# Performance work log

Measured on AMD Instinct MI355X. Metric: run time of the kernel, lower is better.

## Reference

```python
import jax, jax.numpy as jnp
import numpy as np

B, L, D = 4, 2048, 2048
NH, HD, K = 32, 64, 16
LR = 1.0
EPS = 1e-6


def ln_fwd(x, gamma, beta):
    mu = x.mean(-1, keepdims=True)
    var = jnp.var(x, axis=-1, keepdims=True)
    x_hat = (x - mu) / jnp.sqrt(var + EPS)
    return gamma * x_hat + beta


def ln_fused_l2_bwd(x, target, gamma, beta):
    # grad of 0.5*||LN(x)-target||^2 wrt x (matches LayerNormFunction.backward
    # with grad_output = LN(x) - target)
    d = x.shape[-1]
    mu = x.mean(-1, keepdims=True)
    var = jnp.var(x, axis=-1, keepdims=True)
    std = jnp.sqrt(var + EPS)
    x_hat = (x - mu) / std
    y = gamma * x_hat + beta
    g = (y - target) * gamma
    return (d * g - g.sum(-1, keepdims=True) - x_hat * (g * x_hat).sum(-1, keepdims=True)) / (d * std)


def setup_inputs() -> dict:
    key = jax.random.key(0)
    ks = jax.random.split(key, 12)
    s = 0.02
    return {
        "hidden_states": jax.random.normal(ks[0], (B, L, D), jnp.float32),
        "Wq": jax.random.normal(ks[1], (D, D), jnp.float32) * s,
        "Wk": jax.random.normal(ks[2], (D, D), jnp.float32) * s,
        "Wv": jax.random.normal(ks[3], (D, D), jnp.float32) * s,
        "Wo": jax.random.normal(ks[4], (D, D), jnp.float32) * s,
        "linear_weight": jax.random.normal(ks[5], (NH, 1, D), jnp.float32) * s,
        "linear_bias": jnp.zeros((NH, 1), jnp.float32),
        "ln_weight": jnp.ones((NH, HD), jnp.float32),
        "ln_bias": jnp.zeros((NH, HD), jnp.float32),
        "W1_init": jax.random.normal(ks[6], (NH, HD, HD), jnp.float32) * s,
        "b1_init": jnp.zeros((NH, 1, HD), jnp.float32),
    }


def reference(hidden_states, Wq, Wk, Wv, Wo, linear_weight, linear_bias,
              ln_weight, ln_bias, W1_init, b1_init):
    Bq, Lq, Dq = hidden_states.shape
    n_chunk = Lq // K

    def split(x):  # [B,L,D] -> [B,NH,n_chunk,K,HD]
        return x.reshape(Bq, n_chunk, K, NH, HD).transpose(0, 3, 1, 2, 4)

    XC = split(hidden_states @ Wq.T)
    XB = split(hidden_states @ Wk.T)
    XA = split(hidden_states @ Wv.T)

    # inner-loop learning-rate coefficient: [B,NH,n_chunk,K,1]
    X = hidden_states.reshape(Bq, n_chunk, K, Dq)
    ilr = jnp.einsum('bnkd,hd->bhnk', X, linear_weight[:, 0, :]) + linear_bias[:, 0][None, :, None, None]
    ilr_gated = jax.nn.sigmoid(ilr)[..., None]
    token_idx = 1.0 / jnp.arange(1, K + 1, dtype=hidden_states.dtype)
    coeff = (LR * token_idx).reshape(1, 1, 1, K, 1) * ilr_gated / HD

    ln_w = ln_weight.reshape(1, NH, 1, HD)
    ln_b = ln_bias.reshape(1, NH, 1, HD)
    mask = jnp.tril(jnp.ones((K, K), hidden_states.dtype))

    W1 = jnp.broadcast_to(W1_init[None], (Bq, NH, HD, HD))
    b1 = jnp.broadcast_to(b1_init[None], (Bq, NH, 1, HD))

    def step(carry, inp):
        W1, b1 = carry
        xc, xb, xa, co = inp  # [B,NH,K,HD], co: [B,NH,K,1]
        Z1 = xb @ W1 + b1
        grad = ln_fused_l2_bwd(Z1, xa - xb, ln_w, ln_b)  # [B,NH,K,HD]
        Attn = mask * jnp.einsum('bhkf,bhjf->bhkj', xc, xb)
        E = mask * co.transpose(0, 1, 3, 2)  # E[i,j] = coeff_j * (j<=i)
        b1_bar = b1 - E @ grad
        Z1_bar = xc @ W1 - (Attn * E) @ grad + b1_bar
        W1_new = W1 - jnp.einsum('bhkf,bhkg->bhfg', co * xb, grad)
        b1_new = b1 - (co * grad).sum(-2, keepdims=True)
        out = xc + ln_fwd(Z1_bar, ln_w, ln_b)
        return (W1_new, b1_new), out

    xs = (XC.transpose(2, 0, 1, 3, 4), XB.transpose(2, 0, 1, 3, 4),
          XA.transpose(2, 0, 1, 3, 4), coeff.transpose(2, 0, 1, 3, 4))
    (_, _), outs = jax.lax.scan(step, (W1, b1), xs)
    # outs: [n_chunk,B,NH,K,HD] -> [B,L,D]
    XCW = outs.transpose(1, 0, 3, 2, 4).reshape(Bq, Lq, Dq)
    return XCW @ Wo.T
```

## Files before the change

kernel.cpp:

```cpp
#include <hip/hip_runtime.h>


typedef __attribute__((ext_vector_type(4))) float float4v;
typedef __attribute__((ext_vector_type(8))) __bf16 bf16x8;
typedef __attribute__((ext_vector_type(4))) short short4v;
typedef __attribute__((ext_vector_type(4))) unsigned int uint4v;
typedef __attribute__((ext_vector_type(2))) unsigned int uint2v;

__device__ __forceinline__ unsigned short f2bf(float f) {
  unsigned int u = __builtin_bit_cast(unsigned int, f);
  u += 0x7FFFu + ((u >> 16) & 1u);
  return (unsigned short)(u >> 16);
}
__device__ __forceinline__ float bf2f(unsigned short s) {
  unsigned int u = ((unsigned int)s) << 16;
  return __builtin_bit_cast(float, u);
}
__device__ __forceinline__ void lds_load16(const void* g, void* l) {
  __builtin_amdgcn_global_load_lds((const __attribute__((address_space(1))) void*)g,
                                   (__attribute__((address_space(3))) void*)l, 16, 0, 0);
}

__device__ __forceinline__ void store_out(float* p, float v) { *p = v; }
__device__ __forceinline__ void store_out(unsigned short* p, float v) { *p = f2bf(v); }

template <int CTRL>
__device__ __forceinline__ float dppmov(float x) {
  return __builtin_bit_cast(
      float, __builtin_amdgcn_update_dpp(0, __builtin_bit_cast(int, x), CTRL, 0xF, 0xF, true));
}
__device__ __forceinline__ float red16(float x) {
  x += dppmov<0xB1>(x);
  x += dppmov<0x4E>(x);
  x += dppmov<0x124>(x);
  x += dppmov<0x128>(x);
  return x;
}
__device__ __forceinline__ unsigned int cvtpk_bf16(float lo, float hi) {
  unsigned int r;
  asm("v_cvt_pk_bf16_f32 %0, %1, %2" : "=v"(r) : "v"(lo), "v"(hi));
  return r;
}

template <typename OUT>
__global__ __launch_bounds__(256) void gemm_bt(
    const unsigned short* __restrict__ A, const unsigned short* __restrict__ B,
    OUT* __restrict__ C, int M, int N, int K) {
  __shared__ unsigned short sA[128 * 32];
  __shared__ unsigned short sB[128 * 32];
  const int tid = threadIdx.x;
  const int wave = tid >> 6;
  const int lane = tid & 63;
  const int quad = lane >> 4;
  const int l15 = lane & 15;
  const int wm = (wave >> 1) * 64;
  const int wn = (wave & 1) * 64;
  const int bm = blockIdx.y * 128;
  const int bn = blockIdx.x * 128;

  float4v acc[4][4];
#pragma unroll
  for (int i = 0; i < 4; ++i)
#pragma unroll
    for (int j = 0; j < 4; ++j) acc[i][j] = (float4v){0.f, 0.f, 0.f, 0.f};

  const int srow = tid >> 2;
  const int scol = (tid & 3) * 8;
  const unsigned short* aptr = A + (size_t)(bm + srow) * K + scol;
  const unsigned short* bptr = B + (size_t)(bn + srow) * K + scol;
  unsigned short* sAw0 = &sA[wave * 512];
  unsigned short* sAw1 = &sA[2048 + wave * 512];
  unsigned short* sBw0 = &sB[wave * 512];
  unsigned short* sBw1 = &sB[2048 + wave * 512];
  const size_t astep = (size_t)64 * K;

  for (int kt = 0; kt < K; kt += 32) {
    __syncthreads();
    lds_load16(aptr + kt, sAw0);
    lds_load16(aptr + kt + astep, sAw1);
    lds_load16(bptr + kt, sBw0);
    lds_load16(bptr + kt + astep, sBw1);
    __syncthreads();
    bf16x8 af[4], bf[4];
#pragma unroll
    for (int i = 0; i < 4; ++i)
      af[i] = *(const bf16x8*)&sA[(wm + i * 16 + l15) * 32 + quad * 8];
#pragma unroll
    for (int j = 0; j < 4; ++j)
      bf[j] = *(const bf16x8*)&sB[(wn + j * 16 + l15) * 32 + quad * 8];
#pragma unroll
    for (int i = 0; i < 4; ++i)
#pragma unroll
      for (int j = 0; j < 4; ++j)
        acc[i][j] = __builtin_amdgcn_mfma_f32_16x16x32_bf16(af[i], bf[j], acc[i][j], 0, 0, 0);
  }

#pragma unroll
  for (int i = 0; i < 4; ++i) {
    const int row0 = bm + wm + i * 16 + quad * 4;
#pragma unroll
    for (int j = 0; j < 4; ++j) {
      const int col = bn + wn + j * 16 + l15;
#pragma unroll
      for (int r = 0; r < 4; ++r)
        store_out(&C[(size_t)(row0 + r) * N + col], acc[i][j][r]);
    }
  }
}

__global__ __launch_bounds__(256) void f32_to_bf16_k(const float* __restrict__ s,
                                                     unsigned short* __restrict__ d, int n) {
  const int i = (blockIdx.x * 256 + threadIdx.x) * 8;
  if (i >= n) return;
  const float4v a = *(const float4v*)(s + i);
  const float4v b = *(const float4v*)(s + i + 4);
  uint4v o;
  o[0] = (unsigned int)f2bf(a[0]) | ((unsigned int)f2bf(a[1]) << 16);
  o[1] = (unsigned int)f2bf(a[2]) | ((unsigned int)f2bf(a[3]) << 16);
  o[2] = (unsigned int)f2bf(b[0]) | ((unsigned int)f2bf(b[1]) << 16);
  o[3] = (unsigned int)f2bf(b[2]) | ((unsigned int)f2bf(b[3]) << 16);
  *(uint4v*)(d + i) = o;
}

__global__ __launch_bounds__(256) void coeff_k(const unsigned short* __restrict__ ilr,
                                               const float* __restrict__ lb,
                                               float* __restrict__ coeff) {
  const int gid = blockIdx.x * 256 + threadIdx.x;
  const int row = gid >> 5;
  const int h = gid & 31;
  const float v = bf2f(ilr[row * 128 + h]) + lb[h];
  const float sig = 1.0f / (1.0f + __expf(-v));
  const int b = row >> 11;
  const int pos = row & 2047;
  const int cc = pos >> 4;
  const int k = pos & 15;
  coeff[((((size_t)b * 32 + h) * 128 + cc) << 4) + k] = sig / (64.0f * (float)(k + 1));
}

__global__ __launch_bounds__(64, 1) void ttt_scan(
    const unsigned short* __restrict__ XC, const unsigned short* __restrict__ XB,
    const unsigned short* __restrict__ XA, const float* __restrict__ coeff,
    const float* __restrict__ lnw, const float* __restrict__ lnb,
    const float* __restrict__ W1i, const float* __restrict__ b1i,
    unsigned short* __restrict__ XCW) {
  const int b = blockIdx.x >> 5;
  const int h = blockIdx.x & 31;
  const int lane = threadIdx.x;
  const int quad = lane >> 4;
  const int l15 = lane & 15;

  constexpr int LDW = 88;
  __shared__ unsigned short sW1[64 * LDW];
  __shared__ unsigned short sXC[16 * LDW];
  __shared__ unsigned short sXB[16 * LDW];
  __shared__ unsigned short sXA[16 * LDW];

  float gam[4], bet[4];
#pragma unroll
  for (int nt = 0; nt < 4; ++nt) {
    gam[nt] = lnw[h * 64 + nt * 16 + l15];
    bet[nt] = lnb[h * 64 + nt * 16 + l15];
  }
  float4v W1r[16];
#pragma unroll
  for (int mt = 0; mt < 4; ++mt)
#pragma unroll
    for (int nt = 0; nt < 4; ++nt) {
      float4v v;
#pragma unroll
      for (int r = 0; r < 4; ++r)
        v[r] = W1i[(size_t)h * 4096 + (size_t)(mt * 16 + quad * 4 + r) * 64 + nt * 16 + l15];
      W1r[mt * 4 + nt] = v;
    }
  float b1v[4];
#pragma unroll
  for (int nt = 0; nt < 4; ++nt) b1v[nt] = b1i[h * 64 + nt * 16 + l15];

  const int srow = lane >> 2;
  const int scol = (lane & 3) * 16;
  const size_t hdoff = (size_t)h * 64;
  const size_t browoff = (size_t)b * 2048;
  const float* cobase = coeff + (((size_t)b * 32 + h) * 128) * 16;
  const float inv64 = 1.0f / 64.0f;
  const float4v zero4 = {0.f, 0.f, 0.f, 0.f};

  uint4v pxc0, pxc1, pxb0, pxb1, pxa0, pxa1;
  float4v pcof;
  {
    const size_t goff = (browoff + (size_t)srow) * 2048 + hdoff + scol;
    pxc0 = *(const uint4v*)(XC + goff);
    pxc1 = *(const uint4v*)(XC + goff + 8);
    pxb0 = *(const uint4v*)(XB + goff);
    pxb1 = *(const uint4v*)(XB + goff + 8);
    pxa0 = *(const uint4v*)(XA + goff);
    pxa1 = *(const uint4v*)(XA + goff + 8);
    pcof = *(const float4v*)(cobase + quad * 4);
  }

  for (int c = 0; c < 128; ++c) {
    const uint4v xc0 = pxc0, xc1 = pxc1, xb0 = pxb0, xb1 = pxb1, xa0 = pxa0, xa1 = pxa1;
    const float4v cof = pcof;
    {
      const int cn = (c < 127) ? c + 1 : 127;
      const size_t goff = (browoff + (size_t)(cn * 16 + srow)) * 2048 + hdoff + scol;
      pxc0 = *(const uint4v*)(XC + goff);
      pxc1 = *(const uint4v*)(XC + goff + 8);
      pxb0 = *(const uint4v*)(XB + goff);
      pxb1 = *(const uint4v*)(XB + goff + 8);
      pxa0 = *(const uint4v*)(XA + goff);
      pxa1 = *(const uint4v*)(XA + goff + 8);
      pcof = *(const float4v*)(cobase + (size_t)cn * 16 + quad * 4);
    }

    *(uint4v*)&sXC[srow * LDW + scol] = xc0;
    *(uint4v*)&sXC[srow * LDW + scol + 8] = xc1;
    *(uint4v*)&sXB[srow * LDW + scol] = xb0;
    *(uint4v*)&sXB[srow * LDW + scol + 8] = xb1;
    *(uint4v*)&sXA[srow * LDW + scol] = xa0;
    *(uint4v*)&sXA[srow * LDW + scol + 8] = xa1;

#pragma unroll
    for (int mt = 0; mt < 4; ++mt)
#pragma unroll
      for (int nt = 0; nt < 4; ++nt) {
        const float4v w = W1r[mt * 4 + nt];
        uint2v p;
        p[0] = cvtpk_bf16(w[0], w[1]);
        p[1] = cvtpk_bf16(w[2], w[3]);
        *(uint2v*)&sW1[(nt * 16 + l15) * LDW + mt * 16 + quad * 4] = p;
      }

    bf16x8 xbf[2], xcf[2];
#pragma unroll
    for (int hh = 0; hh < 2; ++hh) {
      xbf[hh] = *(const bf16x8*)&sXB[l15 * LDW + hh * 32 + quad * 8];
      xcf[hh] = *(const bf16x8*)&sXC[l15 * LDW + hh * 32 + quad * 8];
    }
    bf16x8 w1f[4][2];
#pragma unroll
    for (int nt = 0; nt < 4; ++nt)
#pragma unroll
      for (int hh = 0; hh < 2; ++hh)
        w1f[nt][hh] = *(const bf16x8*)&sW1[(nt * 16 + l15) * LDW + hh * 32 + quad * 8];

    float4v at = __builtin_amdgcn_mfma_f32_16x16x32_bf16(xbf[0], xcf[0], zero4, 0, 0, 0);
    at = __builtin_amdgcn_mfma_f32_16x16x32_bf16(xbf[1], xcf[1], at, 0, 0, 0);

    float4v z[4];
#pragma unroll
    for (int nt = 0; nt < 4; ++nt) {
      float4v t = __builtin_amdgcn_mfma_f32_16x16x32_bf16(xbf[0], w1f[nt][0], zero4, 0, 0, 0);
      t = __builtin_amdgcn_mfma_f32_16x16x32_bf16(xbf[1], w1f[nt][1], t, 0, 0, 0);
#pragma unroll
      for (int r = 0; r < 4; ++r) t[r] += b1v[nt];
      z[nt] = t;
    }

    float s1[4], s2[4];
#pragma unroll
    for (int r = 0; r < 4; ++r) {
      s1[r] = red16(z[0][r] + z[1][r] + z[2][r] + z[3][r]);
      s2[r] = red16(z[0][r] * z[0][r] + z[1][r] * z[1][r] + z[2][r] * z[2][r] +
                    z[3][r] * z[3][r]);
    }
    float mu[4], rstd[4];
#pragma unroll
    for (int r = 0; r < 4; ++r) {
      mu[r] = s1[r] * inv64;
      const float var = s2[r] * inv64 - mu[r] * mu[r];
      rstd[r] = rsqrtf(var + 1e-6f);
    }
    float xh[4][4], gg[4][4];
#pragma unroll
    for (int nt = 0; nt < 4; ++nt)
#pragma unroll
      for (int r = 0; r < 4; ++r) {
        const float xhat = (z[nt][r] - mu[r]) * rstd[r];
        xh[nt][r] = xhat;
        const float y = gam[nt] * xhat + bet[nt];
        const int toff = (quad * 4 + r) * LDW + nt * 16 + l15;
        const float tgt = bf2f(sXA[toff]) - bf2f(sXB[toff]);
        gg[nt][r] = (y - tgt) * gam[nt];
      }
    float sg[4], sgx[4];
#pragma unroll
    for (int r = 0; r < 4; ++r) {
      sg[r] = red16(gg[0][r] + gg[1][r] + gg[2][r] + gg[3][r]);
      sgx[r] = red16(gg[0][r] * xh[0][r] + gg[1][r] * xh[1][r] + gg[2][r] * xh[2][r] +
                     gg[3][r] * xh[3][r]);
    }
    float grad[4][4];
    short4v gradb[4];
#pragma unroll
    for (int nt = 0; nt < 4; ++nt)
#pragma unroll
      for (int r = 0; r < 4; ++r) {
        grad[nt][r] = (64.0f * gg[nt][r] - sg[r] - xh[nt][r] * sgx[r]) * (rstd[r] * inv64);
        gradb[nt][r] = (short)f2bf(grad[nt][r]);
      }

    short4v m1f;
#pragma unroll
    for (int jj = 0; jj < 4; ++jj) {
      const int k = quad * 4 + jj;
      const float e = (k <= l15) ? cof[jj] : 0.0f;
      m1f[jj] = (short)f2bf(-(at[jj] + 1.0f) * e);
    }

#pragma unroll
    for (int nt = 0; nt < 4; ++nt) {
      float4v t = __builtin_amdgcn_mfma_f32_16x16x32_bf16(xcf[0], w1f[nt][0], zero4, 0, 0, 0);
      t = __builtin_amdgcn_mfma_f32_16x16x32_bf16(xcf[1], w1f[nt][1], t, 0, 0, 0);
      t = __builtin_amdgcn_mfma_f32_16x16x16bf16_1k(m1f, gradb[nt], t, 0, 0, 0);
#pragma unroll
      for (int r = 0; r < 4; ++r) t[r] += b1v[nt];
      z[nt] = t;
    }

#pragma unroll
    for (int r = 0; r < 4; ++r) {
      s1[r] = red16(z[0][r] + z[1][r] + z[2][r] + z[3][r]);
      s2[r] = red16(z[0][r] * z[0][r] + z[1][r] * z[1][r] + z[2][r] * z[2][r] +
                    z[3][r] * z[3][r]);
    }
#pragma unroll
    for (int r = 0; r < 4; ++r) {
      mu[r] = s1[r] * inv64;
      const float var = s2[r] * inv64 - mu[r] * mu[r];
      rstd[r] = rsqrtf(var + 1e-6f);
    }
#pragma unroll
    for (int nt = 0; nt < 4; ++nt)
#pragma unroll
      for (int r = 0; r < 4; ++r) {
        const float xhat = (z[nt][r] - mu[r]) * rstd[r];
        const float y = gam[nt] * xhat + bet[nt];
        const float o = bf2f(sXC[(quad * 4 + r) * LDW + nt * 16 + l15]) + y;
        XCW[(browoff + (size_t)(c * 16 + quad * 4 + r)) * 2048 + hdoff + nt * 16 + l15] = f2bf(o);
      }

#pragma unroll
    for (int nt = 0; nt < 4; ++nt) {
      float pb = cof[0] * grad[nt][0] + cof[1] * grad[nt][1] + cof[2] * grad[nt][2] +
                 cof[3] * grad[nt][3];
      pb += __shfl_xor(pb, 16);
      pb += __shfl_xor(pb, 32);
      b1v[nt] -= pb;
    }

#pragma unroll
    for (int mt = 0; mt < 4; ++mt) {
      short4v caf;
#pragma unroll
      for (int jj = 0; jj < 4; ++jj)
        caf[jj] = (short)f2bf(-cof[jj] * bf2f(sXB[(quad * 4 + jj) * LDW + mt * 16 + l15]));
#pragma unroll
      for (int nt = 0; nt < 4; ++nt)
        W1r[mt * 4 + nt] =
            __builtin_amdgcn_mfma_f32_16x16x16bf16_1k(caf, gradb[nt], W1r[mt * 4 + nt], 0, 0, 0);
    }
  }
}

extern "C" void kernel_launch(void* const* d_in, const int* in_sizes, int n_in,
                              void* d_out, int out_size, void* d_ws, size_t ws_size,
                              hipStream_t stream) {
  const float* hs = (const float*)d_in[0];
  const float* Wq = (const float*)d_in[1];
  const float* Wk = (const float*)d_in[2];
  const float* Wv = (const float*)d_in[3];
  const float* Wo = (const float*)d_in[4];
  const float* lw = (const float*)d_in[5];
  const float* lb = (const float*)d_in[6];
  const float* lnw = (const float*)d_in[7];
  const float* lnb = (const float*)d_in[8];
  const float* W1i = (const float*)d_in[9];
  const float* b1i = (const float*)d_in[10];
  float* out = (float*)d_out;
  char* ws = (char*)d_ws;

  unsigned short* hsb = (unsigned short*)(ws);
  unsigned short* wqb = (unsigned short*)(ws + 33554432);
  unsigned short* wkb = (unsigned short*)(ws + 41943040);
  unsigned short* wvb = (unsigned short*)(ws + 50331648);
  unsigned short* wob = (unsigned short*)(ws + 58720256);
  unsigned short* lwb = (unsigned short*)(ws + 67108864);
  unsigned short* XCb = (unsigned short*)(ws + 67633152);
  unsigned short* XBb = (unsigned short*)(ws + 101187584);
  unsigned short* XAb = (unsigned short*)(ws + 134742016);
  unsigned short* ilrb = (unsigned short*)(ws + 168296448);
  float* coeff = (float*)(ws + 170393600);

  f32_to_bf16_k<<<8192, 256, 0, stream>>>(hs, hsb, 16777216);
  f32_to_bf16_k<<<2048, 256, 0, stream>>>(Wq, wqb, 4194304);
  f32_to_bf16_k<<<2048, 256, 0, stream>>>(Wk, wkb, 4194304);
  f32_to_bf16_k<<<2048, 256, 0, stream>>>(Wv, wvb, 4194304);
  f32_to_bf16_k<<<2048, 256, 0, stream>>>(Wo, wob, 4194304);
  hipMemsetAsync(lwb, 0, 524288, stream);
  f32_to_bf16_k<<<32, 256, 0, stream>>>(lw, lwb, 65536);

  dim3 blk(256);
  dim3 gbig(16, 64);
  gemm_bt<unsigned short><<<gbig, blk, 0, stream>>>(hsb, wqb, XCb, 8192, 2048, 2048);
  gemm_bt<unsigned short><<<gbig, blk, 0, stream>>>(hsb, wkb, XBb, 8192, 2048, 2048);
  gemm_bt<unsigned short><<<gbig, blk, 0, stream>>>(hsb, wvb, XAb, 8192, 2048, 2048);
  gemm_bt<unsigned short><<<dim3(1, 64), blk, 0, stream>>>(hsb, lwb, ilrb, 8192, 128, 2048);
  coeff_k<<<1024, 256, 0, stream>>>(ilrb, lb, coeff);
  ttt_scan<<<128, 64, 0, stream>>>(XCb, XBb, XAb, coeff, lnw, lnb, W1i, b1i, hsb);
  gemm_bt<float><<<gbig, blk, 0, stream>>>(hsb, wob, out, 8192, 2048, 2048);
}
```

Measured before the change: 1.012 ms.

## Split TTT scan across four waves per head with LDS cross-wave reductions

The sequential TTT scan kernel now runs each (batch, head) block with four waves instead of one. Each wave owns a 16-column slice of the 64-wide feature dimension, so W1 state and MFMA work are divided four ways. LayerNorm row statistics are combined across waves through a small shared-memory reduction buffer, which adds three block barriers per chunk. Input tiles are double-buffered in LDS. The aim is to shorten the latency-bound serial chain per chunk, at the cost of barrier synchronisation overhead.

```diff
diff --git a/kernel.cpp b/kernel.cpp
--- a/kernel.cpp
+++ b/kernel.cpp
@@ -2,6 +2,7 @@
 
 
 typedef __attribute__((ext_vector_type(4))) float float4v;
+typedef __attribute__((ext_vector_type(2))) float float2v;
 typedef __attribute__((ext_vector_type(8))) __bf16 bf16x8;
 typedef __attribute__((ext_vector_type(4))) short short4v;
 typedef __attribute__((ext_vector_type(4))) unsigned int uint4v;
@@ -40,6 +41,11 @@
   unsigned int r;
   asm("v_cvt_pk_bf16_f32 %0, %1, %2" : "=v"(r) : "v"(lo), "v"(hi));
   return r;
+}
+__device__ __forceinline__ void bar_sync() {
+  asm volatile("s_waitcnt lgkmcnt(0)" ::: "memory");
+  __builtin_amdgcn_s_barrier();
+  asm volatile("" ::: "memory");
 }
 
 template <typename OUT>
@@ -137,7 +143,7 @@
   coeff[((((size_t)b * 32 + h) * 128 + cc) << 4) + k] = sig / (64.0f * (float)(k + 1));
 }
 
-__global__ __launch_bounds__(64, 1) void ttt_scan(
+__global__ __launch_bounds__(256, 1) void ttt_scan(
     const unsigned short* __restrict__ XC, const unsigned short* __restrict__ XB,
     const unsigned short* __restrict__ XA, const float* __restrict__ coeff,
     const float* __restrict__ lnw, const float* __restrict__ lnb,
@@ -145,160 +151,154 @@
     unsigned short* __restrict__ XCW) {
   const int b = blockIdx.x >> 5;
   const int h = blockIdx.x & 31;
-  const int lane = threadIdx.x;
+  const int tid = threadIdx.x;
+  const int wave = tid >> 6;
+  const int lane = tid & 63;
   const int quad = lane >> 4;
   const int l15 = lane & 15;
 
   constexpr int LDW = 88;
-  __shared__ unsigned short sW1[64 * LDW];
-  __shared__ unsigned short sXC[16 * LDW];
-  __shared__ unsigned short sXB[16 * LDW];
-  __shared__ unsigned short sXA[16 * LDW];
-
-  float gam[4], bet[4];
-#pragma unroll
-  for (int nt = 0; nt < 4; ++nt) {
-    gam[nt] = lnw[h * 64 + nt * 16 + l15];
-    bet[nt] = lnb[h * 64 + nt * 16 + l15];
-  }
-  float4v W1r[16];
-#pragma unroll
-  for (int mt = 0; mt < 4; ++mt)
-#pragma unroll
-    for (int nt = 0; nt < 4; ++nt) {
-      float4v v;
-#pragma unroll
-      for (int r = 0; r < 4; ++r)
-        v[r] = W1i[(size_t)h * 4096 + (size_t)(mt * 16 + quad * 4 + r) * 64 + nt * 16 + l15];
-      W1r[mt * 4 + nt] = v;
-    }
-  float b1v[4];
-#pragma unroll
-  for (int nt = 0; nt < 4; ++nt) b1v[nt] = b1i[h * 64 + nt * 16 + l15];
-
-  const int srow = lane >> 2;
-  const int scol = (lane & 3) * 16;
+  __shared__ __attribute__((aligned(16))) unsigned short sXC[2][16 * LDW];
+  __shared__ __attribute__((aligned(16))) unsigned short sXB[2][16 * LDW];
+  __shared__ __attribute__((aligned(16))) unsigned short sXA[2][16 * LDW];
+  __shared__ __attribute__((aligned(16))) unsigned short sW1[64 * LDW];
+  __shared__ __attribute__((aligned(16))) float sRed[3][16][8];
+
+  const int fcol = wave * 16 + l15;
+  const float gam = lnw[h * 64 + fcol];
+  const float bet = lnb[h * 64 + fcol];
+
+  float4v W1r[4];
+#pragma unroll
+  for (int mt = 0; mt < 4; ++mt) {
+    float4v v;
+#pragma unroll
+    for (int r = 0; r < 4; ++r)
+      v[r] = W1i[(size_t)h * 4096 + (size_t)(mt * 16 + quad * 4 + r) * 64 + fcol];
+    W1r[mt] = v;
+  }
+  float b1v = b1i[h * 64 + fcol];
+
+#pragma unroll
+  for (int mt = 0; mt < 4; ++mt) {
+    uint2v p;
+    p[0] = cvtpk_bf16(W1r[mt][0], W1r[mt][1]);
+    p[1] = cvtpk_bf16(W1r[mt][2], W1r[mt][3]);
+    *(uint2v*)&sW1[(size_t)fcol * LDW + mt * 16 + quad * 4] = p;
+  }
+
+  const int u = tid & 127;
+  const int grow = u >> 3;
+  const int gcol = (u & 7) * 8;
   const size_t hdoff = (size_t)h * 64;
   const size_t browoff = (size_t)b * 2048;
   const float* cobase = coeff + (((size_t)b * 32 + h) * 128) * 16;
   const float inv64 = 1.0f / 64.0f;
   const float4v zero4 = {0.f, 0.f, 0.f, 0.f};
 
-  uint4v pxc0, pxc1, pxb0, pxb1, pxa0, pxa1;
+  uint4v pA = {0, 0, 0, 0}, pB = {0, 0, 0, 0};
   float4v pcof;
   {
-    const size_t goff = (browoff + (size_t)srow) * 2048 + hdoff + scol;
-    pxc0 = *(const uint4v*)(XC + goff);
-    pxc1 = *(const uint4v*)(XC + goff + 8);
-    pxb0 = *(const uint4v*)(XB + goff);
-    pxb1 = *(const uint4v*)(XB + goff + 8);
-    pxa0 = *(const uint4v*)(XA + goff);
-    pxa1 = *(const uint4v*)(XA + goff + 8);
+    const size_t goff = (browoff + (size_t)grow) * 2048 + hdoff + gcol;
+    if (tid < 128) {
+      pA = *(const uint4v*)(XC + goff);
+      pB = *(const uint4v*)(XA + goff);
+    } else {
+      pA = *(const uint4v*)(XB + goff);
+    }
     pcof = *(const float4v*)(cobase + quad * 4);
   }
 
   for (int c = 0; c < 128; ++c) {
-    const uint4v xc0 = pxc0, xc1 = pxc1, xb0 = pxb0, xb1 = pxb1, xa0 = pxa0, xa1 = pxa1;
+    const int buf = c & 1;
+    if (tid < 128) {
+      *(uint4v*)&sXC[buf][grow * LDW + gcol] = pA;
+      *(uint4v*)&sXA[buf][grow * LDW + gcol] = pB;
+    } else {
+      *(uint4v*)&sXB[buf][grow * LDW + gcol] = pA;
+    }
     const float4v cof = pcof;
+    bar_sync();
+
     {
       const int cn = (c < 127) ? c + 1 : 127;
-      const size_t goff = (browoff + (size_t)(cn * 16 + srow)) * 2048 + hdoff + scol;
-      pxc0 = *(const uint4v*)(XC + goff);
-      pxc1 = *(const uint4v*)(XC + goff + 8);
-      pxb0 = *(const uint4v*)(XB + goff);
-      pxb1 = *(const uint4v*)(XB + goff + 8);
-      pxa0 = *(const uint4v*)(XA + goff);
-      pxa1 = *(const uint4v*)(XA + goff + 8);
+      const size_t goff = (browoff + (size_t)(cn * 16 + grow)) * 2048 + hdoff + gcol;
+      if (tid < 128) {
+        pA = *(const uint4v*)(XC + goff);
+        pB = *(const uint4v*)(XA + goff);
+      } else {
+        pA = *(const uint4v*)(XB + goff);
+      }
       pcof = *(const float4v*)(cobase + (size_t)cn * 16 + quad * 4);
     }
 
-    *(uint4v*)&sXC[srow * LDW + scol] = xc0;
-    *(uint4v*)&sXC[srow * LDW + scol + 8] = xc1;
-    *(uint4v*)&sXB[srow * LDW + scol] = xb0;
-    *(uint4v*)&sXB[srow * LDW + scol + 8] = xb1;
-    *(uint4v*)&sXA[srow * LDW + scol] = xa0;
-    *(uint4v*)&sXA[srow * LDW + scol + 8] = xa1;
-
-#pragma unroll
-    for (int mt = 0; mt < 4; ++mt)
-#pragma unroll
-      for (int nt = 0; nt < 4; ++nt) {
-        const float4v w = W1r[mt * 4 + nt];
-        uint2v p;
-        p[0] = cvtpk_bf16(w[0], w[1]);
-        p[1] = cvtpk_bf16(w[2], w[3]);
-        *(uint2v*)&sW1[(nt * 16 + l15) * LDW + mt * 16 + quad * 4] = p;
-      }
-
-    bf16x8 xbf[2], xcf[2];
+    bf16x8 xbf[2], xcf[2], w1f[2];
 #pragma unroll
     for (int hh = 0; hh < 2; ++hh) {
-      xbf[hh] = *(const bf16x8*)&sXB[l15 * LDW + hh * 32 + quad * 8];
-      xcf[hh] = *(const bf16x8*)&sXC[l15 * LDW + hh * 32 + quad * 8];
-    }
-    bf16x8 w1f[4][2];
-#pragma unroll
-    for (int nt = 0; nt < 4; ++nt)
-#pragma unroll
-      for (int hh = 0; hh < 2; ++hh)
-        w1f[nt][hh] = *(const bf16x8*)&sW1[(nt * 16 + l15) * LDW + hh * 32 + quad * 8];
+      xbf[hh] = *(const bf16x8*)&sXB[buf][l15 * LDW + hh * 32 + quad * 8];
+      xcf[hh] = *(const bf16x8*)&sXC[buf][l15 * LDW + hh * 32 + quad * 8];
+      w1f[hh] = *(const bf16x8*)&sW1[(size_t)fcol * LDW + hh * 32 + quad * 8];
+    }
+
+    float4v z = __builtin_amdgcn_mfma_f32_16x16x32_bf16(xbf[0], w1f[0], zero4, 0, 0, 0);
+    z = __builtin_amdgcn_mfma_f32_16x16x32_bf16(xbf[1], w1f[1], z, 0, 0, 0);
+#pragma unroll
+    for (int r = 0; r < 4; ++r) z[r] += b1v;
+
+    float s1p[4], s2p[4];
+#pragma unroll
+    for (int r = 0; r < 4; ++r) {
+      s1p[r] = red16(z[r]);
+      s2p[r] = red16(z[r] * z[r]);
+    }
+    if (l15 == 0) {
+#pragma unroll
+      for (int r = 0; r < 4; ++r)
+        *(float2v*)&sRed[0][quad * 4 + r][wave * 2] = (float2v){s1p[r], s2p[r]};
+    }
 
     float4v at = __builtin_amdgcn_mfma_f32_16x16x32_bf16(xbf[0], xcf[0], zero4, 0, 0, 0);
     at = __builtin_amdgcn_mfma_f32_16x16x32_bf16(xbf[1], xcf[1], at, 0, 0, 0);
 
-    float4v z[4];
-#pragma unroll
-    for (int nt = 0; nt < 4; ++nt) {
-      float4v t = __builtin_amdgcn_mfma_f32_16x16x32_bf16(xbf[0], w1f[nt][0], zero4, 0, 0, 0);
-      t = __builtin_amdgcn_mfma_f32_16x16x32_bf16(xbf[1], w1f[nt][1], t, 0, 0, 0);
-#pragma unroll
-      for (int r = 0; r < 4; ++r) t[r] += b1v[nt];
-      z[nt] = t;
-    }
-
-    float s1[4], s2[4];
-#pragma unroll
-    for (int r = 0; r < 4; ++r) {
-      s1[r] = red16(z[0][r] + z[1][r] + z[2][r] + z[3][r]);
-      s2[r] = red16(z[0][r] * z[0][r] + z[1][r] * z[1][r] + z[2][r] * z[2][r] +
-                    z[3][r] * z[3][r]);
-    }
+    bar_sync();
+
     float mu[4], rstd[4];
 #pragma unroll
     for (int r = 0; r < 4; ++r) {
-      mu[r] = s1[r] * inv64;
-      const float var = s2[r] * inv64 - mu[r] * mu[r];
-      rstd[r] = rsqrtf(var + 1e-6f);
-    }
-    float xh[4][4], gg[4][4];
-#pragma unroll
-    for (int nt = 0; nt < 4; ++nt)
-#pragma unroll
-      for (int r = 0; r < 4; ++r) {
-        const float xhat = (z[nt][r] - mu[r]) * rstd[r];
-        xh[nt][r] = xhat;
-        const float y = gam[nt] * xhat + bet[nt];
-        const int toff = (quad * 4 + r) * LDW + nt * 16 + l15;
-        const float tgt = bf2f(sXA[toff]) - bf2f(sXB[toff]);
-        gg[nt][r] = (y - tgt) * gam[nt];
-      }
-    float sg[4], sgx[4];
-#pragma unroll
-    for (int r = 0; r < 4; ++r) {
-      sg[r] = red16(gg[0][r] + gg[1][r] + gg[2][r] + gg[3][r]);
-      sgx[r] = red16(gg[0][r] * xh[0][r] + gg[1][r] * xh[1][r] + gg[2][r] * xh[2][r] +
-                     gg[3][r] * xh[3][r]);
-    }
-    float grad[4][4];
-    short4v gradb[4];
-#pragma unroll
-    for (int nt = 0; nt < 4; ++nt)
-#pragma unroll
-      for (int r = 0; r < 4; ++r) {
-        grad[nt][r] = (64.0f * gg[nt][r] - sg[r] - xh[nt][r] * sgx[r]) * (rstd[r] * inv64);
-        gradb[nt][r] = (short)f2bf(grad[nt][r]);
-      }
-
+      const float4v v0 = *(const float4v*)&sRed[0][quad * 4 + r][0];
+      const float4v v1 = *(const float4v*)&sRed[0][quad * 4 + r][4];
+      const float s1 = v0[0] + v0[2] + v1[0] + v1[2];
+      const float s2 = v0[1] + v0[3] + v1[1] + v1[3];
+      mu[r] = s1 * inv64;
+      rstd[r] = rsqrtf(s2 * inv64 - mu[r] * mu[r] + 1e-6f);
+    }
+    float xh[4], gg[4];
+#pragma unroll
+    for (int r = 0; r < 4; ++r) {
+      xh[r] = (z[r] - mu[r]) * rstd[r];
+      const int toff = (quad * 4 + r) * LDW + fcol;
+      const float tgt = bf2f(sXA[buf][toff]) - bf2f(sXB[buf][toff]);
+      gg[r] = (gam * xh[r] + bet - tgt) * gam;
+    }
+    float sgp[4], sgxp[4];
+#pragma unroll
+    for (int r = 0; r < 4; ++r) {
+      sgp[r] = red16(gg[r]);
+      sgxp[r] = red16(gg[r] * xh[r]);
+    }
+    if (l15 == 0) {
+#pragma unroll
+      for (int r = 0; r < 4; ++r)
+        *(float2v*)&sRed[1][quad * 4 + r][wave * 2] = (float2v){sgp[r], sgxp[r]};
+    }
+
+    short4v caf[4];
+#pragma unroll
+    for (int mt = 0; mt < 4; ++mt)
+#pragma unroll
+      for (int jj = 0; jj < 4; ++jj)
+        caf[mt][jj] =
+            (short)f2bf(-cof[jj] * bf2f(sXB[buf][(quad * 4 + jj) * LDW + mt * 16 + l15]));
     short4v m1f;
 #pragma unroll
     for (int jj = 0; jj < 4; ++jj) {
@@ -307,57 +307,69 @@
       m1f[jj] = (short)f2bf(-(at[jj] + 1.0f) * e);
     }
 
-#pragma unroll
-    for (int nt = 0; nt < 4; ++nt) {
-      float4v t = __builtin_amdgcn_mfma_f32_16x16x32_bf16(xcf[0], w1f[nt][0], zero4, 0, 0, 0);
-      t = __builtin_amdgcn_mfma_f32_16x16x32_bf16(xcf[1], w1f[nt][1], t, 0, 0, 0);
-      t = __builtin_amdgcn_mfma_f32_16x16x16bf16_1k(m1f, gradb[nt], t, 0, 0, 0);
-#pragma unroll
-      for (int r = 0; r < 4; ++r) t[r] += b1v[nt];
-      z[nt] = t;
-    }
-
-#pragma unroll
-    for (int r = 0; r < 4; ++r) {
-      s1[r] = red16(z[0][r] + z[1][r] + z[2][r] + z[3][r]);
-      s2[r] = red16(z[0][r] * z[0][r] + z[1][r] * z[1][r] + z[2][r] * z[2][r] +
-                    z[3][r] * z[3][r]);
-    }
-#pragma unroll
-    for (int r = 0; r < 4; ++r) {
-      mu[r] = s1[r] * inv64;
-      const float var = s2[r] * inv64 - mu[r] * mu[r];
-      rstd[r] = rsqrtf(var + 1e-6f);
-    }
-#pragma unroll
-    for (int nt = 0; nt < 4; ++nt)
-#pragma unroll
-      for (int r = 0; r < 4; ++r) {
-        const float xhat = (z[nt][r] - mu[r]) * rstd[r];
-        const float y = gam[nt] * xhat + bet[nt];
-        const float o = bf2f(sXC[(quad * 4 + r) * LDW + nt * 16 + l15]) + y;
-        XCW[(browoff + (size_t)(c * 16 + quad * 4 + r)) * 2048 + hdoff + nt * 16 + l15] = f2bf(o);
-      }
-
-#pragma unroll
-    for (int nt = 0; nt < 4; ++nt) {
-      float pb = cof[0] * grad[nt][0] + cof[1] * grad[nt][1] + cof[2] * grad[nt][2] +
-                 cof[3] * grad[nt][3];
+    bar_sync();
+
+    float grad[4];
+    short4v gradb;
+#pragma unroll
+    for (int r = 0; r < 4; ++r) {
+      const float4v v0 = *(const float4v*)&sRed[1][quad * 4 + r][0];
+      const float4v v1 = *(const float4v*)&sRed[1][quad * 4 + r][4];
+      const float sg = v0[0] + v0[2] + v1[0] + v1[2];
+      const float sgx = v0[1] + v0[3] + v1[1] + v1[3];
+      grad[r] = (64.0f * gg[r] - sg - xh[r] * sgx) * (rstd[r] * inv64);
+      gradb[r] = (short)f2bf(grad[r]);
+    }
+
+    float4v zb = __builtin_amdgcn_mfma_f32_16x16x32_bf16(xcf[0], w1f[0], zero4, 0, 0, 0);
+    zb = __builtin_amdgcn_mfma_f32_16x16x32_bf16(xcf[1], w1f[1], zb, 0, 0, 0);
+    zb = __builtin_amdgcn_mfma_f32_16x16x16bf16_1k(m1f, gradb, zb, 0, 0, 0);
+#pragma unroll
+    for (int r = 0; r < 4; ++r) zb[r] += b1v;
+
+#pragma unroll
+    for (int r = 0; r < 4; ++r) {
+      s1p[r] = red16(zb[r]);
+      s2p[r] = red16(zb[r] * zb[r]);
+    }
+    if (l15 == 0) {
+#pragma unroll
+      for (int r = 0; r < 4; ++r)
+        *(float2v*)&sRed[2][quad * 4 + r][wave * 2] = (float2v){s1p[r], s2p[r]};
+    }
+
+    {
+      float pb = cof[0] * grad[0] + cof[1] * grad[1] + cof[2] * grad[2] + cof[3] * grad[3];
       pb += __shfl_xor(pb, 16);
       pb += __shfl_xor(pb, 32);
-      b1v[nt] -= pb;
+      b1v -= pb;
+    }
+#pragma unroll
+    for (int mt = 0; mt < 4; ++mt)
+      W1r[mt] = __builtin_amdgcn_mfma_f32_16x16x16bf16_1k(caf[mt], gradb, W1r[mt], 0, 0, 0);
+
+    bar_sync();
+
+#pragma unroll
+    for (int r = 0; r < 4; ++r) {
+      const float4v v0 = *(const float4v*)&sRed[2][quad * 4 + r][0];
+      const float4v v1 = *(const float4v*)&sRed[2][quad * 4 + r][4];
+      const float s1 = v0[0] + v0[2] + v1[0] + v1[2];
+      const float s2 = v0[1] + v0[3] + v1[1] + v1[3];
+      const float mu2 = s1 * inv64;
+      const float rstd2 = rsqrtf(s2 * inv64 - mu2 * mu2 + 1e-6f);
+      const float xhat = (zb[r] - mu2) * rstd2;
+      const float y = gam * xhat + bet;
+      const float o = bf2f(sXC[buf][(quad * 4 + r) * LDW + fcol]) + y;
+      XCW[(browoff + (size_t)(c * 16 + quad * 4 + r)) * 2048 + hdoff + fcol] = f2bf(o);
     }
 
 #pragma unroll
     for (int mt = 0; mt < 4; ++mt) {
-      short4v caf;
-#pragma unroll
-      for (int jj = 0; jj < 4; ++jj)
-        caf[jj] = (short)f2bf(-cof[jj] * bf2f(sXB[(quad * 4 + jj) * LDW + mt * 16 + l15]));
-#pragma unroll
-      for (int nt = 0; nt < 4; ++nt)
-        W1r[mt * 4 + nt] =
-            __builtin_amdgcn_mfma_f32_16x16x16bf16_1k(caf, gradb[nt], W1r[mt * 4 + nt], 0, 0, 0);
+      uint2v p;
+      p[0] = cvtpk_bf16(W1r[mt][0], W1r[mt][1]);
+      p[1] = cvtpk_bf16(W1r[mt][2], W1r[mt][3]);
+      *(uint2v*)&sW1[(size_t)fcol * LDW + mt * 16 + quad * 4] = p;
     }
   }
 }
@@ -406,6 +418,6 @@
   gemm_bt<unsigned short><<<gbig, blk, 0, stream>>>(hsb, wvb, XAb, 8192, 2048, 2048);
   gemm_bt<unsigned short><<<dim3(1, 64), blk, 0, stream>>>(hsb, lwb, ilrb, 8192, 128, 2048);
   coeff_k<<<1024, 256, 0, stream>>>(ilrb, lb, coeff);
-  ttt_scan<<<128, 64, 0, stream>>>(XCb, XBb, XAb, coeff, lnw, lnb, W1i, b1i, hsb);
+  ttt_scan<<<128, 256, 0, stream>>>(XCb, XBb, XAb, coeff, lnw, lnb, W1i, b1i, hsb);
   gemm_bt<float><<<gbig, blk, 0, stream>>>(hsb, wob, out, 8192, 2048, 2048);
 }
```

Result: faster. 926.1 us (-8.5%).
